# Optimization experiments

Hardware: AMD Instinct MI355X
Metric: run time of the kernel (lower is better)

The kernel has to match this reference:

```python
import jax, jax.numpy as jnp
import numpy as np

# Dimensions (see shape_source)
B, C, H, W = 8, 3, 256, 256
WIDTH = 32   # FNO width
MODES = 12   # modes1 == modes2
L = 4        # number of FNO layers
GAP = 4      # encoder_de sample_gap
PAD = 9      # trans_net.padding


def _downsample(x):
    # Faithful vectorized form of encoder_de.output: keep indices i % GAP == 0
    # (output size int((N-1)/GAP)+1 == number of multiples of GAP below N).
    return x[:, :, ::GAP, ::GAP]


def _spectral_conv(x, w1, w2):
    # SpectralConv2d: rfft2 -> low-mode complex channel mix -> irfft2
    Hp, Wp = x.shape[-2], x.shape[-1]
    x_ft = jnp.fft.rfft2(x)  # [B, WIDTH, Hp, Wp//2+1] complex64
    out_ft = jnp.zeros((x.shape[0], w1.shape[1], Hp, Wp // 2 + 1), dtype=jnp.complex64)
    out_ft = out_ft.at[:, :, :MODES, :MODES].set(
        jnp.einsum('bixy,ioxy->boxy', x_ft[:, :, :MODES, :MODES], w1))
    out_ft = out_ft.at[:, :, -MODES:, :MODES].set(
        jnp.einsum('bixy,ioxy->boxy', x_ft[:, :, -MODES:, :MODES], w2))
    return jnp.fft.irfft2(out_ft, s=(Hp, Wp))


def _forward(x_en, fc0_w, fc0_b, w1r, w1i, w2r, w2i, pw_w, pw_b,
             fc1_w, fc1_b, fc2_w, fc2_b):
    x_de = _downsample(x_en)
    # fc0 on channels-last, back to channels-first
    x = jnp.einsum('bchw,cd->bdhw', x_en, fc0_w) + fc0_b[None, :, None, None]
    # F.pad(x, [0, PAD, 0, PAD]) pads right/bottom of last two dims
    x = jnp.pad(x, ((0, 0), (0, 0), (0, PAD), (0, PAD)))
    for l in range(L):
        w1 = (w1r[l] + 1j * w1i[l]).astype(jnp.complex64)
        w2 = (w2r[l] + 1j * w2i[l]).astype(jnp.complex64)
        x1 = _spectral_conv(x, w1, w2)
        x2 = jnp.einsum('bihw,oi->bohw', x, pw_w[l]) + pw_b[l][None, :, None, None]
        x = x1 + x2
        if l < L - 1:  # last layer has no activation
            x = jax.nn.gelu(x, approximate=False)  # torch F.gelu default = exact erf
    trans_out = x[..., :-PAD, :-PAD].transpose(0, 2, 3, 1)  # [B,H,W,WIDTH]
    h = jax.nn.gelu(trans_out @ fc1_w + fc1_b, approximate=False)  # [B,H,W,128]
    pred_delta = (h @ fc2_w + fc2_b).transpose(0, 3, 1, 2)          # [B,3,H,W]
    pred = pred_delta + x_en
    pred_de = _downsample(pred)
    return pred_de, x_de, pred, x_en


def setup_inputs() -> dict:
    key = jax.random.key(0)
    ks = jax.random.split(key, 14)
    scale = 1.0 / (WIDTH * WIDTH)
    f32 = jnp.float32
    x_en = jax.random.normal(ks[0], (B, C, H, W), f32)
    ctr = jnp.zeros((B, 1), f32)  # accepted but unused by trans_net.forward
    fc0_w = jax.random.normal(ks[1], (3, WIDTH), f32) * 0.2
    fc0_b = jnp.zeros((WIDTH,), f32)
    # torch.rand(..., dtype=cfloat): uniform [0,1) real and imag parts
    w1r = scale * jax.random.uniform(ks[2], (L, WIDTH, WIDTH, MODES, MODES), f32)
    w1i = scale * jax.random.uniform(ks[3], (L, WIDTH, WIDTH, MODES, MODES), f32)
    w2r = scale * jax.random.uniform(ks[4], (L, WIDTH, WIDTH, MODES, MODES), f32)
    w2i = scale * jax.random.uniform(ks[5], (L, WIDTH, WIDTH, MODES, MODES), f32)
    pw_w = jax.random.normal(ks[6], (L, WIDTH, WIDTH), f32) / np.sqrt(WIDTH)  # 1x1 conv [out,in]
    pw_b = jnp.zeros((L, WIDTH), f32)
    fc1_w = jax.random.normal(ks[7], (WIDTH, 128), f32) / np.sqrt(WIDTH)
    fc1_b = jnp.zeros((128,), f32)
    fc2_w = jax.random.normal(ks[8], (128, 3), f32) / np.sqrt(128.0)
    fc2_b = jnp.zeros((3,), f32)
    return dict(x_en=x_en, ctr=ctr, fc0_w=fc0_w, fc0_b=fc0_b,
                w1r=w1r, w1i=w1i, w2r=w2r, w2i=w2i,
                pw_w=pw_w, pw_b=pw_b, fc1_w=fc1_w, fc1_b=fc1_b,
                fc2_w=fc2_w, fc2_b=fc2_b)


def reference(x_en, ctr, fc0_w, fc0_b, w1r, w1i, w2r, w2i, pw_w, pw_b,
              fc1_w, fc1_b, fc2_w, fc2_b):
    del ctr  # unused in the original trans_net.forward
    return _forward(x_en, fc0_w, fc0_b, w1r, w1i, w2r, w2i, pw_w, pw_b,
                    fc1_w, fc1_b, fc2_w, fc2_b)
```

## Files before the change

kernel.cpp:

```cpp
#include <hip/hip_runtime.h>
#include <math.h>

#define HP 265
#define NPIX 70225
#define ROWF 8480
#define TWO_PI 6.28318530717958647692f

#define OFF_X     0
#define OFF_U     8988800
#define OFF_G     10752640
#define OFF_A     11342464
#define OFF_TFB   12427904
#define OFF_TS    12432512
#define OFF_W1B   12436864
#define OFF_W2B   12438912
#define OFF_PWB   12439936

typedef __attribute__((ext_vector_type(8))) short short8;
typedef __attribute__((ext_vector_type(4))) float f32x4;

__device__ __forceinline__ float gelu_f(float v){
  float x2 = v*v;
  float p  = fmaf(x2, 0.10295597f, 2.30212056f);
  float tn = -v*p;
  float e  = __builtin_amdgcn_exp2f(tn);
  float r  = __builtin_amdgcn_rcpf(1.0f + e);
  return v * r;
}
__device__ __forceinline__ unsigned short f2b(float f){
  unsigned u = __float_as_uint(f);
  u += 0x7FFFu + ((u >> 16) & 1u);
  return (unsigned short)(u >> 16);
}
__device__ __forceinline__ unsigned pk(unsigned short lo, unsigned short hi){
  return (unsigned)lo | ((unsigned)hi << 16);
}

__device__ __forceinline__ void init_body(int idx,
                       unsigned short* __restrict__ Tfb, unsigned short* __restrict__ Ts,
                       unsigned short* __restrict__ w1b, unsigned short* __restrict__ w2b,
                       unsigned short* __restrict__ pwb,
                       const float* __restrict__ fc1w, const float* __restrict__ fc2w,
                       const float* __restrict__ pw_w){
  if (idx < 32*288){
    int m = idx / 288, hc = idx % 288;
    unsigned short v = 0;
    if (m < 26 && hc < 265){
      int k = m >> 1;
      int t = (hc*k) % HP;
      float s, c; sincosf(TWO_PI*(float)t/(float)HP, &s, &c);
      v = f2b((m & 1) ? -s : c);
    }
    Tfb[idx] = v;
  }
  if (idx < 272*32){
    int w = idx >> 5, kap = idx & 31;
    unsigned short v = 0;
    if (w < HP && kap < 24){
      int k = kap >> 1;
      int t = (w*k) % HP;
      float s, c; sincosf(TWO_PI*(float)t/(float)HP, &s, &c);
      const float invN = 1.f/70225.f;
      float val = (!(kap&1)) ? invN*(k==0 ? 1.f : 2.f*c)
                             : ((k==0) ? 0.f : -invN*2.f*s);
      v = f2b(val);
    }
    Ts[idx] = v;
  }
  if (idx < 4096){
    int n = idx >> 5, k = idx & 31;
    w1b[idx] = f2b(fc1w[k*128 + n]);
  }
  if (idx < 2048){
    int n = idx >> 7, k = idx & 127;
    w2b[idx] = (n < 3) ? f2b(fc2w[k*3 + n]) : (unsigned short)0;
  }
  if (idx < 4096)
    pwb[idx] = f2b(pw_w[idx]);
}

__global__ __launch_bounds__(256) void k_fc0(const float* __restrict__ xen,
                                             const float* __restrict__ w0,
                                             const float* __restrict__ b0,
                                             unsigned short* __restrict__ xb,
                                             float* __restrict__ out,
                                             unsigned short* __restrict__ Tfb,
                                             unsigned short* __restrict__ Ts,
                                             unsigned short* __restrict__ w1b,
                                             unsigned short* __restrict__ w2b,
                                             unsigned short* __restrict__ pwb,
                                             const float* __restrict__ fc1w,
                                             const float* __restrict__ fc2w,
                                             const float* __restrict__ pw_w){
  if (blockIdx.x >= 2195){
    init_body((blockIdx.x - 2195)*256 + threadIdx.x, Tfb, Ts, w1b, w2b, pwb,
              fc1w, fc2w, pw_w);
    return;
  }
  int idx = blockIdx.x*256 + threadIdx.x;
  if (idx >= 8*NPIX) return;
  int w = idx % HP; int t = idx / HP; int h = t % HP; int b = t / HP;
  unsigned short o16[32];
  if (h < 256 && w < 256){
    const float* xp = xen + (((size_t)b*3)*256 + h)*256 + w;
    float c0 = xp[0], c1 = xp[65536], c2 = xp[131072];
    #pragma unroll
    for (int d = 0; d < 32; ++d)
      o16[d] = f2b(b0[d] + c0*w0[d] + c1*w0[32+d] + c2*w0[64+d]);
    size_t be = ((size_t)b*3)*65536 + (h<<8) + w;
    out[1769472 + be]          = c0;
    out[1769472 + be + 65536]  = c1;
    out[1769472 + be + 131072] = c2;
    if (((h|w)&3) == 0){
      size_t db = ((size_t)b*3)*4096 + ((h>>2)<<6) + (w>>2);
      out[98304 + db]        = c0;
      out[98304 + db + 4096] = c1;
      out[98304 + db + 8192] = c2;
    }
  } else {
    #pragma unroll
    for (int d = 0; d < 32; ++d) o16[d] = 0;
  }
  uint4* dst = (uint4*)(xb + (size_t)idx*32);
  #pragma unroll
  for (int q = 0; q < 4; ++q)
    dst[q] = make_uint4(pk(o16[8*q],o16[8*q+1]), pk(o16[8*q+2],o16[8*q+3]),
                        pk(o16[8*q+4],o16[8*q+5]), pk(o16[8*q+6],o16[8*q+7]));
}

__global__ __launch_bounds__(256) void k_dftm(const unsigned short* __restrict__ xb,
                                              const unsigned short* __restrict__ Tfb,
                                              float* __restrict__ U32){
  int tid = threadIdx.x;
  int wv = tid>>6, lane = tid&63, lr = lane&15, g = lane>>4, lk = g*8;
  int n0 = blockIdx.x*64;
  int b  = blockIdx.y;
  int n  = n0 + wv*16 + lr;
  const unsigned short* xcol = xb + (size_t)b*HP*ROWF + n;
  f32x4 acc0 = {0.f,0.f,0.f,0.f}, acc1 = {0.f,0.f,0.f,0.f};
  #pragma unroll
  for (int kc = 0; kc < 9; ++kc){
    short8 hv;
    int hb = kc*32 + lk;
    #pragma unroll
    for (int q = 0; q < 8; ++q){
      int h = hb + q;
      hv[q] = (h < HP) ? (short)xcol[(size_t)h*ROWF] : (short)0;
    }
    short8 aT0 = *(const short8*)&Tfb[lr*288 + kc*32 + lk];
    short8 aT1 = *(const short8*)&Tfb[(16+lr)*288 + kc*32 + lk];
    acc0 = __builtin_amdgcn_mfma_f32_16x16x32_bf16(aT0, hv, acc0, 0,0,0);
    acc1 = __builtin_amdgcn_mfma_f32_16x16x32_bf16(aT1, hv, acc1, 0,0,0);
  }
  if (n < 8480){
    #pragma unroll
    for (int r = 0; r < 4; ++r){
      int m0 = g*4 + r;
      U32[((size_t)b*26 + m0)*8480 + n] = acc0[r];
      int m1 = 16 + m0;
      if (m1 < 26) U32[((size_t)b*26 + m1)*8480 + n] = acc1[r];
    }
  }
}

__global__ __launch_bounds__(256) void k_spec(const float* __restrict__ U32,
                                              const float* __restrict__ w1r,
                                              const float* __restrict__ w1i,
                                              const float* __restrict__ w2r,
                                              const float* __restrict__ w2i,
                                              float2* __restrict__ G, int l){
  __shared__ float part[256*25];
  __shared__ float Xs[32*25];
  int j = blockIdx.x;
  int b = blockIdx.y;
  int ws = blockIdx.z;
  int tid = threadIdx.x;
  int wsub = tid >> 5, i = tid & 31;
  int kk   = (j < 12) ? j : (24 - j);
  bool cj  = (j >= 12);
  float xr[12], xi[12];
  #pragma unroll
  for (int k = 0; k < 12; ++k){ xr[k] = 0.f; xi[k] = 0.f; }
  const float* ubr = U32 + ((size_t)(b*26 + 2*kk))*8480;
  for (int w = ws*8 + wsub; w < HP; w += 32){
    int n = w*32 + i;
    float ux = ubr[n];
    float uy = ubr[8480 + n];
    if (cj) uy = -uy;
    float bs, bc; sincosf(-TWO_PI*(float)w/(float)HP, &bs, &bc);
    float pr = 1.f, pi = 0.f;
    #pragma unroll
    for (int k = 0; k < 12; ++k){
      xr[k] = fmaf(ux, pr, fmaf(-uy, pi, xr[k]));
      xi[k] = fmaf(ux, pi, fmaf( uy, pr, xi[k]));
      float npr = pr*bc - pi*bs;
      pi = fmaf(pr, bs, pi*bc);
      pr = npr;
    }
  }
  #pragma unroll
  for (int k = 0; k < 12; ++k){
    part[tid*25 + 2*k]     = xr[k];
    part[tid*25 + 2*k + 1] = xi[k];
  }
  __syncthreads();
  {
    int sg = tid >> 5;
    int ii = tid & 31;
    #pragma unroll
    for (int s0 = 0; s0 < 3; ++s0){
      int s = sg*3 + s0;
      float acc = 0.f;
      #pragma unroll
      for (int wq = 0; wq < 8; ++wq) acc += part[(wq*32 + ii)*25 + s];
      Xs[ii*25 + s] = acc;
    }
  }
  __syncthreads();
  int ky = (j < 12) ? j : (j - 12);
  const float* wr = (j < 12) ? w1r : w2r;
  const float* wi = (j < 12) ? w1i : w2i;
  float2* Gp = G + (size_t)ws*73728;
  for (int p = tid; p < 384; p += 256){
    int o = p / 12, kx = p % 12;
    size_t wbase = (size_t)l*147456 + (size_t)o*144 + (size_t)ky*12 + kx;
    float gr = 0.f, gi = 0.f;
    #pragma unroll 4
    for (int i2 = 0; i2 < 32; ++i2){
      float xvr = Xs[i2*25 + 2*kx];
      float xvi = Xs[i2*25 + 2*kx + 1];
      float a = wr[wbase + (size_t)i2*4608];
      float c = wi[wbase + (size_t)i2*4608];
      gr += xvr*a - xvi*c;
      gi += xvr*c + xvi*a;
    }
    Gp[((size_t)(b*32 + o)*24 + j)*12 + kx] = make_float2(gr, gi);
  }
}

__global__ __launch_bounds__(320) void k_idft_h(const float2* __restrict__ G,
                                                unsigned short* __restrict__ A16){
  __shared__ float2 gs[288];
  int bo = blockIdx.x;
  for (int i = threadIdx.x; i < 288; i += 320){
    float2 g0 = G[(size_t)bo*288 + i];
    float2 g1 = G[73728 + (size_t)bo*288 + i];
    float2 g2 = G[2*73728 + (size_t)bo*288 + i];
    float2 g3 = G[3*73728 + (size_t)bo*288 + i];
    gs[i] = make_float2(g0.x+g1.x+g2.x+g3.x, g0.y+g1.y+g2.y+g3.y);
  }
  __syncthreads();
  int h = threadIdx.x;
  if (h >= HP) return;
  float ar[12], ai[12];
  #pragma unroll
  for (int k = 0; k < 12; ++k){ ar[k] = 0.f; ai[k] = 0.f; }
  for (int j = 0; j < 24; ++j){
    int ky = (j < 12) ? j : (241 + j);
    int t = (ky*h) % HP;
    float s, c; sincosf(TWO_PI*(float)t/(float)HP, &s, &c);
    #pragma unroll
    for (int k = 0; k < 12; ++k){
      float2 g = gs[j*12 + k];
      ar[k] = fmaf(g.x, c, fmaf(-g.y, s, ar[k]));
      ai[k] = fmaf(g.x, s, fmaf( g.y, c, ai[k]));
    }
  }
  int b = bo >> 5, o = bo & 31;
  unsigned short o16[32];
  #pragma unroll
  for (int k = 0; k < 12; ++k){ o16[2*k] = f2b(ar[k]); o16[2*k+1] = f2b(ai[k]); }
  #pragma unroll
  for (int k = 24; k < 32; ++k) o16[k] = 0;
  uint4* ap = (uint4*)(A16 + (((size_t)(b*HP + h))*32 + o)*32);
  #pragma unroll
  for (int q = 0; q < 4; ++q)
    ap[q] = make_uint4(pk(o16[8*q],o16[8*q+1]), pk(o16[8*q+2],o16[8*q+3]),
                       pk(o16[8*q+4],o16[8*q+5]), pk(o16[8*q+6],o16[8*q+7]));
}

__global__ __launch_bounds__(256) void k_final(const unsigned short* __restrict__ A16,
                                               const unsigned short* __restrict__ Tsyn,
                                               const unsigned short* __restrict__ pwb,
                                               const float* __restrict__ pw_b,
                                               unsigned short* __restrict__ xb, int l){
  int tid = threadIdx.x;
  int wv = tid>>6, lane = tid&63, lr = lane&15, g = lane>>4, lk = g*8;
  int h = blockIdx.x*4 + wv;
  int b = blockIdx.y;
  int z = blockIdx.z;
  if (h >= HP) return;
  const unsigned short* arow = A16 + (size_t)(b*HP + h)*1024;
  short8 aA0 = *(const short8*)&arow[lr*32 + lk];
  short8 aA1 = *(const short8*)&arow[(16+lr)*32 + lk];
  short8 aP0 = *(const short8*)&pwb[l*1024 + lr*32 + lk];
  short8 aP1 = *(const short8*)&pwb[l*1024 + (16+lr)*32 + lk];
  float4 vb0 = *(const float4*)&pw_b[l*32 + g*4];
  float4 vb1 = *(const float4*)&pw_b[l*32 + 16 + g*4];
  unsigned short* xrow = xb + (size_t)(b*HP + h)*ROWF;
  const f32x4 z4 = {0.f,0.f,0.f,0.f};
  int wt0 = z ? 9 : 0, wt1 = z ? 17 : 9;
  for (int wt = wt0; wt < wt1; ++wt){
    int w = wt*16 + lr;
    short8 bT = *(const short8*)&Tsyn[(size_t)w*32 + lk];
    short8 bX = *(const short8*)&xrow[(size_t)w*32 + lk];
    f32x4 a0 = __builtin_amdgcn_mfma_f32_16x16x32_bf16(aA0, bT, z4, 0,0,0);
    a0 = __builtin_amdgcn_mfma_f32_16x16x32_bf16(aP0, bX, a0, 0,0,0);
    f32x4 a1 = __builtin_amdgcn_mfma_f32_16x16x32_bf16(aA1, bT, z4, 0,0,0);
    a1 = __builtin_amdgcn_mfma_f32_16x16x32_bf16(aP1, bX, a1, 0,0,0);
    if (w < HP){
      float v0[4], v1[4];
      v0[0]=a0[0]+vb0.x; v0[1]=a0[1]+vb0.y; v0[2]=a0[2]+vb0.z; v0[3]=a0[3]+vb0.w;
      v1[0]=a1[0]+vb1.x; v1[1]=a1[1]+vb1.y; v1[2]=a1[2]+vb1.z; v1[3]=a1[3]+vb1.w;
      if (l < 3){
        #pragma unroll
        for (int r = 0; r < 4; ++r){ v0[r] = gelu_f(v0[r]); v1[r] = gelu_f(v1[r]); }
      }
      *(uint2*)&xrow[(size_t)w*32 + g*4] =
          make_uint2(pk(f2b(v0[0]),f2b(v0[1])), pk(f2b(v0[2]),f2b(v0[3])));
      *(uint2*)&xrow[(size_t)w*32 + 16 + g*4] =
          make_uint2(pk(f2b(v1[0]),f2b(v1[1])), pk(f2b(v1[2]),f2b(v1[3])));
    }
  }
}

__global__ __launch_bounds__(256) void k_head(const unsigned short* __restrict__ xb,
                                              const float* __restrict__ xen,
                                              const unsigned short* __restrict__ w1b,
                                              const float* __restrict__ fc1b,
                                              const unsigned short* __restrict__ w2b,
                                              const float* __restrict__ fc2b,
                                              float* __restrict__ out){
  __shared__ unsigned short Pm[4][2][16*136];
  int tid = threadIdx.x;
  int b = blockIdx.x >> 8, h = blockIdx.x & 255;
  int wv = tid>>6, lane = tid&63, lr = lane&15, g = lane>>4, lk = g*8;
  short8 bf1[8], bf2[4];
  #pragma unroll
  for (int nt = 0; nt < 8; ++nt)
    bf1[nt] = *(const short8*)&w1b[(nt*16+lr)*32 + lk];
  #pragma unroll
  for (int ks = 0; ks < 4; ++ks)
    bf2[ks] = *(const short8*)&w2b[lr*128 + ks*32 + lk];
  float f2c = (lr < 3) ? fc2b[lr] : 0.f;
  const unsigned short* xrow = xb + (size_t)(b*HP + h)*ROWF;
  const f32x4 z4 = {0.f,0.f,0.f,0.f};

  auto STAGE = [&](int m){
    int p0 = (wv*4 + m)*16;
    short8 ax = *(const short8*)&xrow[(size_t)(p0 + lr)*32 + lk];
    f32x4 acc[8];
    #pragma unroll
    for (int nt = 0; nt < 8; ++nt)
      acc[nt] = __builtin_amdgcn_mfma_f32_16x16x32_bf16(bf1[nt], ax, z4, 0,0,0);
    unsigned short* P = Pm[wv][m & 1];
    #pragma unroll
    for (int nt = 0; nt < 8; ++nt){
      float4 bb = *(const float4*)&fc1b[nt*16 + g*4];
      float h0 = gelu_f(acc[nt][0] + bb.x);
      float h1 = gelu_f(acc[nt][1] + bb.y);
      float h2 = gelu_f(acc[nt][2] + bb.z);
      float h3 = gelu_f(acc[nt][3] + bb.w);
      *(uint2*)&P[lr*136 + nt*16 + g*4] =
          make_uint2(pk(f2b(h0),f2b(h1)), pk(f2b(h2),f2b(h3)));
    }
  };
  auto FC2 = [&](int m){
    const unsigned short* P = Pm[wv][m & 1];
    f32x4 a2 = z4;
    #pragma unroll
    for (int ks = 0; ks < 4; ++ks){
      short8 ap = *(const short8*)&P[lr*136 + ks*32 + lk];
      a2 = __builtin_amdgcn_mfma_f32_16x16x32_bf16(ap, bf2[ks], a2, 0,0,0);
    }
    if (lr < 3){
      int p0 = (wv*4 + m)*16;
      size_t base = ((size_t)(b*3 + lr))*65536 + (h<<8) + p0 + g*4;
      float4 xe = *(const float4*)&xen[base];
      float4 pr;
      pr.x = a2[0] + f2c + xe.x;
      pr.y = a2[1] + f2c + xe.y;
      pr.z = a2[2] + f2c + xe.z;
      pr.w = a2[3] + f2c + xe.w;
      *(float4*)&out[196608 + base] = pr;
      if ((h & 3) == 0){
        int w4 = (p0 + g*4) >> 2;
        out[((size_t)(b*3 + lr))*4096 + ((h>>2)<<6) + w4] = pr.x;
      }
    }
  };

  STAGE(0);
  asm volatile("s_waitcnt lgkmcnt(0)" ::: "memory");
  #pragma unroll
  for (int m = 1; m < 4; ++m){
    STAGE(m);
    FC2(m - 1);
    asm volatile("s_waitcnt lgkmcnt(0)" ::: "memory");
  }
  FC2(3);
}

extern "C" void kernel_launch(void* const* d_in, const int* in_sizes, int n_in,
                              void* d_out, int out_size, void* d_ws, size_t ws_size,
                              hipStream_t stream){
  const float* x_en  = (const float*)d_in[0];
  const float* fc0_w = (const float*)d_in[2];
  const float* fc0_b = (const float*)d_in[3];
  const float* w1r   = (const float*)d_in[4];
  const float* w1i   = (const float*)d_in[5];
  const float* w2r   = (const float*)d_in[6];
  const float* w2i   = (const float*)d_in[7];
  const float* pw_w  = (const float*)d_in[8];
  const float* pw_b  = (const float*)d_in[9];
  const float* fc1_w = (const float*)d_in[10];
  const float* fc1_b = (const float*)d_in[11];
  const float* fc2_w = (const float*)d_in[12];
  const float* fc2_b = (const float*)d_in[13];
  float* out = (float*)d_out;
  float* ws  = (float*)d_ws;

  unsigned short* xb  = (unsigned short*)(ws + OFF_X);
  float*  U32         = ws + OFF_U;
  float2* G           = (float2*)(ws + OFF_G);
  unsigned short* A16 = (unsigned short*)(ws + OFF_A);
  unsigned short* Tfb = (unsigned short*)(ws + OFF_TFB);
  unsigned short* Ts  = (unsigned short*)(ws + OFF_TS);
  unsigned short* w1b = (unsigned short*)(ws + OFF_W1B);
  unsigned short* w2b = (unsigned short*)(ws + OFF_W2B);
  unsigned short* pwb = (unsigned short*)(ws + OFF_PWB);

  k_fc0<<<2231, 256, 0, stream>>>(x_en, fc0_w, fc0_b, xb, out,
                                  Tfb, Ts, w1b, w2b, pwb, fc1_w, fc2_w, pw_w);
  for (int l = 0; l < 4; ++l){
    k_dftm<<<dim3(133,8), 256, 0, stream>>>(xb, Tfb, U32);
    k_spec<<<dim3(24,8,4), 256, 0, stream>>>(U32, w1r, w1i, w2r, w2i, G, l);
    k_idft_h<<<256, 320, 0, stream>>>(G, A16);
    k_final<<<dim3(67,8,2), 256, 0, stream>>>(A16, Ts, pwb, pw_b, xb, l);
  }
  k_head<<<2048, 256, 0, stream>>>(xb, x_en, w1b, fc1_b, w2b, fc2_b, out);
}
```

Baseline: 303.3 us.

## Use hardware bf16 pack conversion and split idft_h and head grids

After: 299.9 us. No clear change (-1.1%).

```diff
diff --git a/kernel.cpp b/kernel.cpp
--- a/kernel.cpp
+++ b/kernel.cpp
@@ -31,6 +31,11 @@
   unsigned u = __float_as_uint(f);
   u += 0x7FFFu + ((u >> 16) & 1u);
   return (unsigned short)(u >> 16);
+}
+__device__ __forceinline__ unsigned cvtpk(float lo, float hi){
+  unsigned r;
+  asm("v_cvt_pk_bf16_f32 %0, %1, %2" : "=v"(r) : "v"(lo), "v"(hi));
+  return r;
 }
 __device__ __forceinline__ unsigned pk(unsigned short lo, unsigned short hi){
   return (unsigned)lo | ((unsigned)hi << 16);
@@ -100,13 +105,13 @@
   int idx = blockIdx.x*256 + threadIdx.x;
   if (idx >= 8*NPIX) return;
   int w = idx % HP; int t = idx / HP; int h = t % HP; int b = t / HP;
-  unsigned short o16[32];
+  float o32[32];
   if (h < 256 && w < 256){
     const float* xp = xen + (((size_t)b*3)*256 + h)*256 + w;
     float c0 = xp[0], c1 = xp[65536], c2 = xp[131072];
     #pragma unroll
     for (int d = 0; d < 32; ++d)
-      o16[d] = f2b(b0[d] + c0*w0[d] + c1*w0[32+d] + c2*w0[64+d]);
+      o32[d] = b0[d] + c0*w0[d] + c1*w0[32+d] + c2*w0[64+d];
     size_t be = ((size_t)b*3)*65536 + (h<<8) + w;
     out[1769472 + be]          = c0;
     out[1769472 + be + 65536]  = c1;
@@ -119,13 +124,13 @@
     }
   } else {
     #pragma unroll
-    for (int d = 0; d < 32; ++d) o16[d] = 0;
+    for (int d = 0; d < 32; ++d) o32[d] = 0.f;
   }
   uint4* dst = (uint4*)(xb + (size_t)idx*32);
   #pragma unroll
   for (int q = 0; q < 4; ++q)
-    dst[q] = make_uint4(pk(o16[8*q],o16[8*q+1]), pk(o16[8*q+2],o16[8*q+3]),
-                        pk(o16[8*q+4],o16[8*q+5]), pk(o16[8*q+6],o16[8*q+7]));
+    dst[q] = make_uint4(cvtpk(o32[8*q],o32[8*q+1]),   cvtpk(o32[8*q+2],o32[8*q+3]),
+                        cvtpk(o32[8*q+4],o32[8*q+5]), cvtpk(o32[8*q+6],o32[8*q+7]));
 }
 
 __global__ __launch_bounds__(256) void k_dftm(const unsigned short* __restrict__ xb,
@@ -250,7 +255,8 @@
     gs[i] = make_float2(g0.x+g1.x+g2.x+g3.x, g0.y+g1.y+g2.y+g3.y);
   }
   __syncthreads();
-  int h = threadIdx.x;
+  if (threadIdx.x >= 133) return;
+  int h = blockIdx.y*133 + threadIdx.x;
   if (h >= HP) return;
   float ar[12], ai[12];
   #pragma unroll
@@ -267,16 +273,12 @@
     }
   }
   int b = bo >> 5, o = bo & 31;
-  unsigned short o16[32];
-  #pragma unroll
-  for (int k = 0; k < 12; ++k){ o16[2*k] = f2b(ar[k]); o16[2*k+1] = f2b(ai[k]); }
-  #pragma unroll
-  for (int k = 24; k < 32; ++k) o16[k] = 0;
   uint4* ap = (uint4*)(A16 + (((size_t)(b*HP + h))*32 + o)*32);
   #pragma unroll
-  for (int q = 0; q < 4; ++q)
-    ap[q] = make_uint4(pk(o16[8*q],o16[8*q+1]), pk(o16[8*q+2],o16[8*q+3]),
-                       pk(o16[8*q+4],o16[8*q+5]), pk(o16[8*q+6],o16[8*q+7]));
+  for (int q = 0; q < 3; ++q)
+    ap[q] = make_uint4(cvtpk(ar[4*q],   ai[4*q]),   cvtpk(ar[4*q+1], ai[4*q+1]),
+                       cvtpk(ar[4*q+2], ai[4*q+2]), cvtpk(ar[4*q+3], ai[4*q+3]));
+  ap[3] = make_uint4(0u, 0u, 0u, 0u);
 }
 
 __global__ __launch_bounds__(256) void k_final(const unsigned short* __restrict__ A16,
@@ -317,9 +319,9 @@
         for (int r = 0; r < 4; ++r){ v0[r] = gelu_f(v0[r]); v1[r] = gelu_f(v1[r]); }
       }
       *(uint2*)&xrow[(size_t)w*32 + g*4] =
-          make_uint2(pk(f2b(v0[0]),f2b(v0[1])), pk(f2b(v0[2]),f2b(v0[3])));
+          make_uint2(cvtpk(v0[0],v0[1]), cvtpk(v0[2],v0[3]));
       *(uint2*)&xrow[(size_t)w*32 + 16 + g*4] =
-          make_uint2(pk(f2b(v1[0]),f2b(v1[1])), pk(f2b(v1[2]),f2b(v1[3])));
+          make_uint2(cvtpk(v1[0],v1[1]), cvtpk(v1[2],v1[3]));
     }
   }
 }
@@ -331,9 +333,10 @@
                                               const unsigned short* __restrict__ w2b,
                                               const float* __restrict__ fc2b,
                                               float* __restrict__ out){
-  __shared__ unsigned short Pm[4][2][16*136];
+  __shared__ unsigned short Pm[4][16*136];
   int tid = threadIdx.x;
-  int b = blockIdx.x >> 8, h = blockIdx.x & 255;
+  int bh = blockIdx.x >> 1, half = blockIdx.x & 1;
+  int b = bh >> 8, h = bh & 255;
   int wv = tid>>6, lane = tid&63, lr = lane&15, g = lane>>4, lk = g*8;
   short8 bf1[8], bf2[4];
   #pragma unroll
@@ -344,16 +347,16 @@
     bf2[ks] = *(const short8*)&w2b[lr*128 + ks*32 + lk];
   float f2c = (lr < 3) ? fc2b[lr] : 0.f;
   const unsigned short* xrow = xb + (size_t)(b*HP + h)*ROWF;
+  unsigned short* P = Pm[wv];
   const f32x4 z4 = {0.f,0.f,0.f,0.f};
-
-  auto STAGE = [&](int m){
-    int p0 = (wv*4 + m)*16;
+  #pragma unroll
+  for (int m = 0; m < 2; ++m){
+    int p0 = (wv*4 + half*2 + m)*16;
     short8 ax = *(const short8*)&xrow[(size_t)(p0 + lr)*32 + lk];
     f32x4 acc[8];
     #pragma unroll
     for (int nt = 0; nt < 8; ++nt)
       acc[nt] = __builtin_amdgcn_mfma_f32_16x16x32_bf16(bf1[nt], ax, z4, 0,0,0);
-    unsigned short* P = Pm[wv][m & 1];
     #pragma unroll
     for (int nt = 0; nt < 8; ++nt){
       float4 bb = *(const float4*)&fc1b[nt*16 + g*4];
@@ -362,11 +365,10 @@
       float h2 = gelu_f(acc[nt][2] + bb.z);
       float h3 = gelu_f(acc[nt][3] + bb.w);
       *(uint2*)&P[lr*136 + nt*16 + g*4] =
-          make_uint2(pk(f2b(h0),f2b(h1)), pk(f2b(h2),f2b(h3)));
-    }
-  };
-  auto FC2 = [&](int m){
-    const unsigned short* P = Pm[wv][m & 1];
+          make_uint2(cvtpk(h0,h1), cvtpk(h2,h3));
+    }
+    asm volatile("s_waitcnt lgkmcnt(0)" ::: "memory");
+    __builtin_amdgcn_sched_barrier(0);
     f32x4 a2 = z4;
     #pragma unroll
     for (int ks = 0; ks < 4; ++ks){
@@ -374,7 +376,6 @@
       a2 = __builtin_amdgcn_mfma_f32_16x16x32_bf16(ap, bf2[ks], a2, 0,0,0);
     }
     if (lr < 3){
-      int p0 = (wv*4 + m)*16;
       size_t base = ((size_t)(b*3 + lr))*65536 + (h<<8) + p0 + g*4;
       float4 xe = *(const float4*)&xen[base];
       float4 pr;
@@ -388,17 +389,7 @@
         out[((size_t)(b*3 + lr))*4096 + ((h>>2)<<6) + w4] = pr.x;
       }
     }
-  };
-
-  STAGE(0);
-  asm volatile("s_waitcnt lgkmcnt(0)" ::: "memory");
-  #pragma unroll
-  for (int m = 1; m < 4; ++m){
-    STAGE(m);
-    FC2(m - 1);
-    asm volatile("s_waitcnt lgkmcnt(0)" ::: "memory");
-  }
-  FC2(3);
+  }
 }
 
 extern "C" void kernel_launch(void* const* d_in, const int* in_sizes, int n_in,
@@ -435,8 +426,8 @@
   for (int l = 0; l < 4; ++l){
     k_dftm<<<dim3(133,8), 256, 0, stream>>>(xb, Tfb, U32);
     k_spec<<<dim3(24,8,4), 256, 0, stream>>>(U32, w1r, w1i, w2r, w2i, G, l);
-    k_idft_h<<<256, 320, 0, stream>>>(G, A16);
+    k_idft_h<<<dim3(256,2), 320, 0, stream>>>(G, A16);
     k_final<<<dim3(67,8,2), 256, 0, stream>>>(A16, Ts, pwb, pw_b, xb, l);
   }
-  k_head<<<2048, 256, 0, stream>>>(xb, x_en, w1b, fc1_b, w2b, fc2_b, out);
-}
+  k_head<<<4096, 256, 0, stream>>>(xb, x_en, w1b, fc1_b, w2b, fc2_b, out);
+}
```
